# Kernel tuning notes

Measured on AMD Instinct MI355X. Metric: run time of the kernel, lower is better.

## Reference

```python
import jax, jax.numpy as jnp
import numpy as np
from jax import lax

# SLAYER neuron / simulation constants (from netParams)
THETA = 10.0       # spike threshold
TAU_SR = 10.0      # synaptic (PSP) time constant
TAU_REF = 1.0      # refractory time constant
SCALE_REF = 2.0    # refractory scale
TAU_RHO = 1.0      # surrogate-gradient width (unused in fwd)
K_PSP = 32         # truncation length of SRM alpha kernel
K_REF = 16         # truncation length of refractory kernel

_t = np.arange(K_PSP, dtype=np.float64)
PSP_KERN = jnp.asarray((_t / TAU_SR) * np.exp(1.0 - _t / TAU_SR), jnp.float32)  # [K_PSP]
_tr = np.arange(1, K_REF + 1, dtype=np.float64)
REF_KERN = jnp.asarray(-SCALE_REF * THETA * (_tr / TAU_REF) * np.exp(1.0 - _tr / TAU_REF), jnp.float32)  # [K_REF]


def psp(x):
    """Causal temporal FIR filter with SRM alpha kernel; x: [..., T]."""
    sh = x.shape
    T = sh[-1]
    flat = x.reshape(-1, 1, T)                       # [B*, 1, T]
    k = PSP_KERN[::-1][None, None, :]                # correlation kernel (reversed)
    y = lax.conv_general_dilated(flat, k, (1,), [(K_PSP - 1, 0)])
    return y.reshape(sh)


def spike(u):
    """Threshold with refractory feedback, sequential over time. u: [..., T]."""
    uT = jnp.moveaxis(u, -1, 0)                      # [T, ...]
    buf0 = jnp.zeros(u.shape[:-1] + (K_REF,), u.dtype)

    def step(buf, ut):
        v = ut + buf[..., 0]
        s = (v >= THETA).astype(u.dtype)
        buf = jnp.concatenate([buf[..., 1:], jnp.zeros_like(buf[..., :1])], -1)
        buf = buf + s[..., None] * REF_KERN
        return buf, s

    _, sT = lax.scan(step, buf0, uT)
    return jnp.moveaxis(sT, 0, -1)


def conv_t(x, w, stride, pad):
    """2D conv applied independently per timestep. x: [N,C,H,W,T], w: [Co,C,kh,kw]."""
    N, C, H, W, T = x.shape
    xt = jnp.moveaxis(x, -1, 1).reshape(N * T, C, H, W)
    y = lax.conv_general_dilated(xt, w, (stride, stride), [(pad, pad), (pad, pad)])
    Co, Ho, Wo = y.shape[1], y.shape[2], y.shape[3]
    return jnp.moveaxis(y.reshape(N, T, Co, Ho, Wo), 1, -1)


def pool_t(x):
    """SLAYER sum-pool 2x2/s2 with weight 1.1*theta/kernel_area. x: [N,C,H,W,T]."""
    s = lax.reduce_window(x, np.float32(0.0), lax.add, (1, 1, 2, 2, 1), (1, 1, 2, 2, 1), 'VALID')
    return s * np.float32(1.1 * THETA / 4.0)


def setup_inputs() -> dict:
    key = jax.random.key(0)
    ks = jax.random.split(key, 5)
    spikeInput = (jax.random.uniform(ks[0], (4, 2, 256, 256, 50)) < 0.02).astype(jnp.float32)
    w1 = jax.random.normal(ks[1], (8, 2, 5, 5), jnp.float32) * 2.0
    w2 = jax.random.normal(ks[2], (16, 8, 3, 3), jnp.float32) * 1.5
    w3 = jax.random.normal(ks[3], (32, 16, 3, 3), jnp.float32) * 1.5
    w_fc = jax.random.normal(ks[4], (2, 32, 8, 8), jnp.float32) * 0.3
    return {"spikeInput": spikeInput, "w1": w1, "w2": w2, "w3": w3, "w_fc": w_fc}


def reference(spikeInput, w1, w2, w3, w_fc):
    x = spike(conv_t(psp(spikeInput), w1, 2, 1))   # [4,8,127,127,50]
    x = spike(pool_t(psp(x)))                      # [4,8,63,63,50]
    x = spike(conv_t(psp(x), w2, 2, 1))            # [4,16,32,32,50]
    x = spike(pool_t(psp(x)))                      # [4,16,16,16,50]
    x = spike(conv_t(psp(x), w3, 2, 1))            # [4,32,8,8,50]
    u = psp(x)
    out = jnp.einsum('ochw,nchwt->not', w_fc, u)   # dense over (C,H,W)
    return spike(out[:, :, None, None, :])         # [4,2,1,1,50]
```

## Files before the change

### kernel.cpp

```cpp
#include <hip/hip_runtime.h>
#include <cmath>

struct K32 { float k[32]; };
struct K16 { float k[16]; };

#define THETA 10.0f

template <int CIN, int COUT, int KK, int HIN, int WIN, int S1H, int S1W,
          int S2H, int S2W>
__global__ __launch_bounds__(256)
void conv_pps_kernel(const float* __restrict__ x, const float* __restrict__ w,
                     float* __restrict__ s2out, K32 pk, K16 rk) {
  constexpr int WT = 4;
  constexpr int SW = 8;
  constexpr int XR = 2 * (WT - 1) + KK;
  constexpr int GROUPS = (S1W + SW - 1) / SW;
  constexpr int NROW = COUT * 2 * SW;
  constexpr int T0 = 39;
  __shared__ float lds[NROW * 51];
  const int tid = threadIdx.x;
  const int wave = tid >> 6;
  const int lane = tid & 63;
  const int group = blockIdx.x % GROUPS;
  const int rest = blockIdx.x / GROUPS;
  const int hop = rest % S2H;
  const int n = rest / S2H;
  const int ho_off = wave & 1;
  const int wo_half = wave >> 1;
  const int ho = 2 * hop + ho_off;
  const int wo0 = group * SW + wo_half * WT;
  const int tt = lane < 50 ? lane : 49;

  float acc[COUT][WT] = {};
  for (int c = 0; c < CIN; ++c) {
#pragma unroll
    for (int kh = 0; kh < KK; ++kh) {
      const int hi = 2 * ho + kh - 1;
      if ((unsigned)hi >= (unsigned)HIN) continue;
      float xr[XR];
#pragma unroll
      for (int i = 0; i < XR; ++i) {
        const int wi = 2 * wo0 - 1 + i;
        xr[i] = ((unsigned)wi < (unsigned)WIN)
                    ? x[(((size_t)(n * CIN + c) * HIN + hi) * WIN + wi) * 50 + tt]
                    : 0.f;
      }
#pragma unroll
      for (int co = 0; co < COUT; ++co)
#pragma unroll
        for (int kw = 0; kw < KK; ++kw) {
          const float wv = w[((co * CIN + c) * KK + kh) * KK + kw];
#pragma unroll
          for (int wl = 0; wl < WT; ++wl)
            acc[co][wl] += xr[2 * wl + kw] * wv;
        }
    }
  }
  if (lane < 50) {
#pragma unroll
    for (int co = 0; co < COUT; ++co)
#pragma unroll
      for (int wl = 0; wl < WT; ++wl)
        lds[((co * 2 + ho_off) * SW + wo_half * WT + wl) * 51 + lane] = acc[co][wl];
  }
  __syncthreads();
  {
    const int r = tid & (NROW - 1);
    const int part = tid >> 7;
    const int wol = r & (SW - 1);
    const bool act = (group * SW + wol) < S1W;
    float xs[50];
    if (act) {
      if (part == 0) {
#pragma unroll
        for (int t = 0; t < T0; ++t) xs[t] = lds[r * 51 + t];
      } else {
#pragma unroll
        for (int t = 0; t < 50; ++t) xs[t] = lds[r * 51 + t];
      }
    }
    __syncthreads();
    if (act) {
      if (part == 0) {
        float us[T0];
#pragma unroll
        for (int t = 0; t < 32; ++t) {
          float a = 0.f;
#pragma unroll
          for (int k = 31; k >= 0; --k)
            if (t - k >= 0) a += xs[t - k] * pk.k[k];
          us[t] = a;
        }
#pragma unroll
        for (int t = 32; t < T0; ++t) {
          float a = 0.f;
#pragma unroll
          for (int k = 31; k >= 0; --k)
            a += xs[t - k] * pk.k[k];
          us[t] = a;
        }
        float buf[16];
#pragma unroll
        for (int j = 0; j < 16; ++j) buf[j] = 0.f;
#pragma unroll
        for (int t = 0; t < T0; ++t) {
          float v = us[t] + buf[t & 15];
          buf[t & 15] = 0.f;
          float sp = 0.f;
          if (v >= THETA) {
            sp = 1.f;
#pragma unroll
            for (int j = 0; j < 16; ++j) buf[(t + 1 + j) & 15] += rk.k[j];
          }
          us[t] = sp;
        }
#pragma unroll
        for (int t = 0; t < 32; ++t) {
          float a = 0.f;
#pragma unroll
          for (int k = 31; k >= 0; --k)
            if (t - k >= 0) a += us[t - k] * pk.k[k];
          lds[r * 51 + t] = a;
        }
#pragma unroll
        for (int t = 32; t < T0; ++t) {
          float a = 0.f;
#pragma unroll
          for (int k = 31; k >= 0; --k)
            a += us[t - k] * pk.k[k];
          lds[r * 51 + t] = a;
        }
      } else {
        float us[50];
#pragma unroll
        for (int t = 0; t < 32; ++t) {
          float a = 0.f;
#pragma unroll
          for (int k = 31; k >= 0; --k)
            if (t - k >= 0) a += xs[t - k] * pk.k[k];
          us[t] = a;
        }
#pragma unroll
        for (int t = 32; t < 50; ++t) {
          float a = 0.f;
#pragma unroll
          for (int k = 31; k >= 0; --k)
            a += xs[t - k] * pk.k[k];
          us[t] = a;
        }
        float buf[16];
#pragma unroll
        for (int j = 0; j < 16; ++j) buf[j] = 0.f;
#pragma unroll
        for (int t = 0; t < 50; ++t) {
          float v = us[t] + buf[t & 15];
          buf[t & 15] = 0.f;
          float sp = 0.f;
          if (v >= THETA) {
            sp = 1.f;
#pragma unroll
            for (int j = 0; j < 16; ++j) buf[(t + 1 + j) & 15] += rk.k[j];
          }
          us[t] = sp;
        }
#pragma unroll
        for (int t = T0; t < 50; ++t) {
          float a = 0.f;
#pragma unroll
          for (int k = 31; k >= 0; --k)
            a += us[t - k] * pk.k[k];
          lds[r * 51 + t] = a;
        }
      }
    }
  }
  __syncthreads();
  if (tid < COUT * (SW / 2)) {
    const int co = tid / (SW / 2);
    const int wpl = tid % (SW / 2);
    const int wop = group * (SW / 2) + wpl;
    if (wop < S2W) {
      const int r00 = (co * 16 + 2 * wpl) * 51;
      const int r01 = (co * 16 + 2 * wpl + 1) * 51;
      const int r10 = (co * 16 + 8 + 2 * wpl) * 51;
      const int r11 = (co * 16 + 8 + 2 * wpl + 1) * 51;
      float* orow = s2out + (((size_t)(n * COUT + co) * S2H + hop) * S2W + wop) * 50;
      float buf[16];
#pragma unroll
      for (int j = 0; j < 16; ++j) buf[j] = 0.f;
      float prev = 0.f;
#pragma unroll
      for (int t = 0; t < 50; ++t) {
        const float u0 = (((lds[r00 + t] + lds[r01 + t]) + lds[r10 + t]) + lds[r11 + t]) * 2.75f;
        float v = u0 + buf[t & 15];
        buf[t & 15] = 0.f;
        float sp = 0.f;
        if (v >= THETA) {
          sp = 1.f;
#pragma unroll
          for (int j = 0; j < 16; ++j) buf[(t + 1 + j) & 15] += rk.k[j];
        }
        if (t & 1) *(float2*)(orow + t - 1) = make_float2(prev, sp);
        else prev = sp;
      }
    }
  }
}

template <int CIN, int COUT, int KK, int SW, int WT, int HIN, int WIN,
          int S1H, int S1W, int S2H, int S2W>
__global__ __launch_bounds__(256)
void conv_pps2_kernel(const float* __restrict__ x, const float* __restrict__ w,
                      float* __restrict__ s2out, K32 pk, K16 rk) {
  constexpr int XR = 2 * (WT - 1) + KK;
  constexpr int GROUPS = (S1W + SW - 1) / SW;
  constexpr int NROW = COUT * 2 * SW;
  constexpr int NROWP = COUT * (SW / 2);
  __shared__ float lds[NROW * 51];
  const int tid = threadIdx.x;
  const int wave = tid >> 6;
  const int lane = tid & 63;
  const int group = blockIdx.x % GROUPS;
  const int rest = blockIdx.x / GROUPS;
  const int hop = rest % S2H;
  const int n = rest / S2H;
  const int ho_off = wave & 1;
  const int wo_half = wave >> 1;
  const int ho = 2 * hop + ho_off;
  const int wo0 = group * SW + wo_half * WT;
  const int tt = lane < 50 ? lane : 49;

  float acc[COUT][WT] = {};
  for (int c = 0; c < CIN; ++c) {
#pragma unroll
    for (int kh = 0; kh < KK; ++kh) {
      const int hi = 2 * ho + kh - 1;
      if ((unsigned)hi >= (unsigned)HIN) continue;
      float xr[XR];
#pragma unroll
      for (int i = 0; i < XR; ++i) {
        const int wi = 2 * wo0 - 1 + i;
        xr[i] = ((unsigned)wi < (unsigned)WIN)
                    ? x[(((size_t)(n * CIN + c) * HIN + hi) * WIN + wi) * 50 + tt]
                    : 0.f;
      }
#pragma unroll
      for (int co = 0; co < COUT; ++co)
#pragma unroll
        for (int kw = 0; kw < KK; ++kw) {
          const float wv = w[((co * CIN + c) * KK + kh) * KK + kw];
#pragma unroll
          for (int wl = 0; wl < WT; ++wl)
            acc[co][wl] += xr[2 * wl + kw] * wv;
        }
    }
  }
  if (lane < 50) {
#pragma unroll
    for (int co = 0; co < COUT; ++co)
#pragma unroll
      for (int wl = 0; wl < WT; ++wl)
        lds[((co * 2 + ho_off) * SW + wo_half * WT + wl) * 51 + lane] = acc[co][wl];
  }
  __syncthreads();
  {
    const int r = tid & (NROW - 1);
    const int part = tid >> 7;
    float xs[50];
    if (part == 0) {
#pragma unroll
      for (int t = 0; t < 32; ++t) xs[t] = lds[r * 51 + t];
    } else {
#pragma unroll
      for (int t = 0; t < 50; ++t) xs[t] = lds[r * 51 + t];
    }
    __syncthreads();
    if (part == 0) {
#pragma unroll
      for (int t = 0; t < 32; ++t) {
        float a = 0.f;
#pragma unroll
        for (int k = 31; k >= 0; --k)
          if (t - k >= 0) a += xs[t - k] * pk.k[k];
        lds[r * 51 + t] = a;
      }
    } else {
#pragma unroll
      for (int t = 32; t < 50; ++t) {
        float a = 0.f;
#pragma unroll
        for (int k = 31; k >= 0; --k)
          a += xs[t - k] * pk.k[k];
        lds[r * 51 + t] = a;
      }
    }
  }
  __syncthreads();
  if (tid < NROW) {
    float buf[16];
#pragma unroll
    for (int j = 0; j < 16; ++j) buf[j] = 0.f;
#pragma unroll
    for (int t = 0; t < 50; ++t) {
      float v = lds[tid * 51 + t] + buf[t & 15];
      buf[t & 15] = 0.f;
      float sp = 0.f;
      if (v >= THETA) {
        sp = 1.f;
#pragma unroll
        for (int j = 0; j < 16; ++j) buf[(t + 1 + j) & 15] += rk.k[j];
      }
      lds[tid * 51 + t] = sp;
    }
  }
  __syncthreads();
  {
    const int r = tid & (NROWP - 1);
    const int part = tid >> 5;
    const bool act = part < 2;
    const int co = r / (SW / 2);
    const int wpl = r % (SW / 2);
    const int r00 = ((co * 2) * SW + 2 * wpl) * 51;
    const int r01 = r00 + 51;
    const int r10 = ((co * 2 + 1) * SW + 2 * wpl) * 51;
    const int r11 = r10 + 51;
    float xs[50];
    if (act) {
      if (part == 0) {
#pragma unroll
        for (int t = 0; t < 32; ++t)
          xs[t] = (((lds[r00 + t] + lds[r01 + t]) + lds[r10 + t]) + lds[r11 + t]) * 2.75f;
      } else {
#pragma unroll
        for (int t = 0; t < 50; ++t)
          xs[t] = (((lds[r00 + t] + lds[r01 + t]) + lds[r10 + t]) + lds[r11 + t]) * 2.75f;
      }
    }
    __syncthreads();
    if (act) {
      if (part == 0) {
#pragma unroll
        for (int t = 0; t < 32; ++t) {
          float a = 0.f;
#pragma unroll
          for (int k = 31; k >= 0; --k)
            if (t - k >= 0) a += xs[t - k] * pk.k[k];
          lds[r00 + t] = a;
        }
      } else {
#pragma unroll
        for (int t = 32; t < 50; ++t) {
          float a = 0.f;
#pragma unroll
          for (int k = 31; k >= 0; --k)
            a += xs[t - k] * pk.k[k];
          lds[r00 + t] = a;
        }
      }
    }
  }
  __syncthreads();
  if (tid < NROWP) {
    const int co = tid / (SW / 2);
    const int wpl = tid % (SW / 2);
    const int wop = group * (SW / 2) + wpl;
    if (wop < S2W) {
      const int r00 = ((co * 2) * SW + 2 * wpl) * 51;
      float* orow = s2out + (((size_t)(n * COUT + co) * S2H + hop) * S2W + wop) * 50;
      float buf[16];
#pragma unroll
      for (int j = 0; j < 16; ++j) buf[j] = 0.f;
      float prev = 0.f;
#pragma unroll
      for (int t = 0; t < 50; ++t) {
        float v = lds[r00 + t] + buf[t & 15];
        buf[t & 15] = 0.f;
        float sp = 0.f;
        if (v >= THETA) {
          sp = 1.f;
#pragma unroll
          for (int j = 0; j < 16; ++j) buf[(t + 1 + j) & 15] += rk.k[j];
        }
        if (t & 1) *(float2*)(orow + t - 1) = make_float2(prev, sp);
        else prev = sp;
      }
    }
  }
}

template <int CIN, int COUT, int KK, int WT, int HIN, int WIN, int HOUT, int WOUT>
__global__ __launch_bounds__(256)
void conv_fir_spike_kernel(const float* __restrict__ x, const float* __restrict__ w,
                           float* __restrict__ s, K32 pk, K16 rk) {
  constexpr int XR = 2 * (WT - 1) + KK;
  constexpr int TW = 4 * WT;
  constexpr int GROUPS = (WOUT + TW - 1) / TW;
  constexpr int NROW = COUT * TW;
  __shared__ float lds[NROW * 51];
  const int tid = threadIdx.x;
  const int wave = tid >> 6;
  const int lane = tid & 63;
  const int group = blockIdx.x % GROUPS;
  const int rest = blockIdx.x / GROUPS;
  const int ho = rest % HOUT;
  const int n = rest / HOUT;
  const int wo0 = group * TW + wave * WT;
  const int tt = lane < 50 ? lane : 49;

  float acc[COUT][WT] = {};
  for (int c = 0; c < CIN; ++c) {
#pragma unroll
    for (int kh = 0; kh < KK; ++kh) {
      const int hi = 2 * ho + kh - 1;
      if ((unsigned)hi >= (unsigned)HIN) continue;
      float xr[XR];
#pragma unroll
      for (int i = 0; i < XR; ++i) {
        const int wi = 2 * wo0 - 1 + i;
        xr[i] = ((unsigned)wi < (unsigned)WIN)
                    ? x[(((size_t)(n * CIN + c) * HIN + hi) * WIN + wi) * 50 + tt]
                    : 0.f;
      }
#pragma unroll
      for (int co = 0; co < COUT; ++co)
#pragma unroll
        for (int kw = 0; kw < KK; ++kw) {
          const float wv = w[((co * CIN + c) * KK + kh) * KK + kw];
#pragma unroll
          for (int wl = 0; wl < WT; ++wl)
            acc[co][wl] += xr[2 * wl + kw] * wv;
        }
    }
  }

  if (lane < 50) {
#pragma unroll
    for (int co = 0; co < COUT; ++co)
#pragma unroll
      for (int wl = 0; wl < WT; ++wl)
        lds[(co * TW + wave * WT + wl) * 51 + lane] = acc[co][wl];
  }
  __syncthreads();
  {
    const int r = tid % NROW;
    const int part = tid / NROW;
    const int wol = r % TW;
    const bool act = (part < 2) && (group * TW + wol < WOUT);
    float xs[50];
    if (act) {
      if (part == 0) {
#pragma unroll
        for (int t = 0; t < 25; ++t) xs[t] = lds[r * 51 + t];
      } else {
#pragma unroll
        for (int t = 0; t < 50; ++t) xs[t] = lds[r * 51 + t];
      }
    }
    __syncthreads();
    if (act) {
      if (part == 0) {
#pragma unroll
        for (int t = 0; t < 25; ++t) {
          float a = 0.f;
#pragma unroll
          for (int k = 31; k >= 0; --k)
            if (t - k >= 0) a += xs[t - k] * pk.k[k];
          lds[r * 51 + t] = a;
        }
      } else {
#pragma unroll
        for (int t = 25; t < 50; ++t) {
          float a = 0.f;
#pragma unroll
          for (int k = 31; k >= 0; --k)
            if (t - k >= 0) a += xs[t - k] * pk.k[k];
          lds[r * 51 + t] = a;
        }
      }
    }
  }
  __syncthreads();
  if (tid < NROW) {
    const int co = tid / TW;
    const int wol = tid - co * TW;
    const int wo = group * TW + wol;
    if (wo < WOUT) {
      float* orow = s + (((size_t)(n * COUT + co) * HOUT + ho) * WOUT + wo) * 50;
      float buf[16];
#pragma unroll
      for (int j = 0; j < 16; ++j) buf[j] = 0.f;
      float prev = 0.f;
#pragma unroll
      for (int t = 0; t < 50; ++t) {
        float v = lds[tid * 51 + t] + buf[t & 15];
        buf[t & 15] = 0.f;
        float sp = 0.f;
        if (v >= THETA) {
          sp = 1.f;
#pragma unroll
          for (int j = 0; j < 16; ++j) buf[(t + 1 + j) & 15] += rk.k[j];
        }
        if (t & 1) *(float2*)(orow + t - 1) = make_float2(prev, sp);
        else prev = sp;
      }
    }
  }
}

__global__ __launch_bounds__(512)
void fc_fir_spike_kernel(const float* __restrict__ w, const float* __restrict__ s,
                         float* __restrict__ out, K32 pk, K16 rk) {
  __shared__ float lds[8 * 51];
  const int tid = threadIdx.x;
  const int wave = tid >> 6, lane = tid & 63;
  const int o = wave & 1, n = wave >> 1;
  const int tt = lane < 50 ? lane : 49;
  const float* wrow = w + (size_t)o * 2048;
  const float* ub = s + (size_t)n * 2048 * 50;
  float acc = 0.f;
#pragma unroll 32
  for (int i = 0; i < 2048; ++i) acc += wrow[i] * ub[(size_t)i * 50 + tt];
  if (lane < 50) lds[wave * 51 + lane] = acc;
  __syncthreads();
  {
    const int r = tid & 7;
    const int part = tid >> 3;
    const bool act = part < 2;
    float xs[50];
    if (act) {
      if (part == 0) {
#pragma unroll
        for (int t = 0; t < 25; ++t) xs[t] = lds[r * 51 + t];
      } else {
#pragma unroll
        for (int t = 0; t < 50; ++t) xs[t] = lds[r * 51 + t];
      }
    }
    __syncthreads();
    if (act) {
      if (part == 0) {
#pragma unroll
        for (int t = 0; t < 25; ++t) {
          float a = 0.f;
#pragma unroll
          for (int k = 31; k >= 0; --k)
            if (t - k >= 0) a += xs[t - k] * pk.k[k];
          lds[r * 51 + t] = a;
        }
      } else {
#pragma unroll
        for (int t = 25; t < 50; ++t) {
          float a = 0.f;
#pragma unroll
          for (int k = 31; k >= 0; --k)
            if (t - k >= 0) a += xs[t - k] * pk.k[k];
          lds[r * 51 + t] = a;
        }
      }
    }
  }
  __syncthreads();
  if (tid < 8) {
    float buf[16];
#pragma unroll
    for (int j = 0; j < 16; ++j) buf[j] = 0.f;
#pragma unroll
    for (int t = 0; t < 50; ++t) {
      float v = lds[tid * 51 + t] + buf[t & 15];
      buf[t & 15] = 0.f;
      float sp = 0.f;
      if (v >= THETA) {
        sp = 1.f;
#pragma unroll
        for (int j = 0; j < 16; ++j) buf[(t + 1 + j) & 15] += rk.k[j];
      }
      out[tid * 50 + t] = sp;
    }
  }
}

extern "C" void kernel_launch(void* const* d_in, const int* in_sizes, int n_in,
                              void* d_out, int out_size, void* d_ws, size_t ws_size,
                              hipStream_t stream) {
  const float* xin = (const float*)d_in[0];
  const float* w1  = (const float*)d_in[1];
  const float* w2  = (const float*)d_in[2];
  const float* w3  = (const float*)d_in[3];
  const float* wfc = (const float*)d_in[4];
  float* out = (float*)d_out;

  float* R0 = (float*)d_ws;
  float* R1 = R0 + 26214400;

  K32 pk;
  for (int k = 0; k < 32; ++k)
    pk.k[k] = (float)(((double)k / 10.0) * exp(1.0 - (double)k / 10.0));
  K16 rk;
  for (int j = 0; j < 16; ++j) {
    const double tr = (double)(j + 1);
    rk.k[j] = (float)(-2.0 * 10.0 * tr * exp(1.0 - tr));
  }

  conv_pps_kernel<2, 8, 5, 256, 256, 127, 127, 63, 63>
      <<<4 * 63 * 16, 256, 0, stream>>>(xin, w1, R1, pk, rk);
  conv_pps2_kernel<8, 16, 3, 4, 2, 63, 63, 32, 32, 16, 16>
      <<<4 * 16 * 8, 256, 0, stream>>>(R1, w2, R0, pk, rk);
  conv_fir_spike_kernel<16, 32, 3, 1, 16, 16, 8, 8>
      <<<4 * 8 * 2, 256, 0, stream>>>(R0, w3, R1, pk, rk);
  fc_fir_spike_kernel<<<1, 512, 0, stream>>>(wfc, R1, out, pk, rk);
}
```

Baseline: 464.8 us.

## Split time-domain PSP/spike work across two thread halves via spike bitmask handoff

Before, the second thread half redundantly recomputed the full 50-step PSP and spike scan, while the first half handled steps 0-38. Now part 0 computes steps 0-31 and writes its spike bits to shared memory as a packed mask. Part 1 precomputes PSP for steps 32-49 in parallel, then rebuilds the refractory buffer from that mask and finishes the scan and output PSP. This cuts redundant serial work at the cost of an extra barrier and some shared-memory traffic.

```diff
diff --git a/kernel.cpp b/kernel.cpp
--- a/kernel.cpp
+++ b/kernel.cpp
@@ -16,7 +16,6 @@
   constexpr int XR = 2 * (WT - 1) + KK;
   constexpr int GROUPS = (S1W + SW - 1) / SW;
   constexpr int NROW = COUT * 2 * SW;
-  constexpr int T0 = 39;
   __shared__ float lds[NROW * 51];
   const int tid = threadIdx.x;
   const int wave = tid >> 6;
@@ -73,87 +72,82 @@
     if (act) {
       if (part == 0) {
 #pragma unroll
-        for (int t = 0; t < T0; ++t) xs[t] = lds[r * 51 + t];
+        for (int t = 0; t < 32; ++t) xs[t] = lds[r * 51 + t];
       } else {
 #pragma unroll
         for (int t = 0; t < 50; ++t) xs[t] = lds[r * 51 + t];
       }
     }
     __syncthreads();
-    if (act) {
-      if (part == 0) {
-        float us[T0];
+    float s0[32];
+    float u1[18];
+    if (act) {
+      if (part == 0) {
 #pragma unroll
         for (int t = 0; t < 32; ++t) {
           float a = 0.f;
 #pragma unroll
           for (int k = 31; k >= 0; --k)
             if (t - k >= 0) a += xs[t - k] * pk.k[k];
-          us[t] = a;
-        }
-#pragma unroll
-        for (int t = 32; t < T0; ++t) {
-          float a = 0.f;
-#pragma unroll
-          for (int k = 31; k >= 0; --k)
-            a += xs[t - k] * pk.k[k];
-          us[t] = a;
+          s0[t] = a;
         }
         float buf[16];
 #pragma unroll
         for (int j = 0; j < 16; ++j) buf[j] = 0.f;
-#pragma unroll
-        for (int t = 0; t < T0; ++t) {
-          float v = us[t] + buf[t & 15];
+        unsigned bits = 0u;
+#pragma unroll
+        for (int t = 0; t < 32; ++t) {
+          float v = s0[t] + buf[t & 15];
           buf[t & 15] = 0.f;
           float sp = 0.f;
           if (v >= THETA) {
             sp = 1.f;
+            bits |= (1u << t);
 #pragma unroll
             for (int j = 0; j < 16; ++j) buf[(t + 1 + j) & 15] += rk.k[j];
           }
-          us[t] = sp;
-        }
+          s0[t] = sp;
+        }
+        lds[r * 51 + 50] = __uint_as_float(bits);
+      } else {
+#pragma unroll
+        for (int t = 32; t < 50; ++t) {
+          float a = 0.f;
+#pragma unroll
+          for (int k = 31; k >= 0; --k)
+            a += xs[t - k] * pk.k[k];
+          u1[t - 32] = a;
+        }
+      }
+    }
+    __syncthreads();
+    if (act) {
+      if (part == 0) {
 #pragma unroll
         for (int t = 0; t < 32; ++t) {
           float a = 0.f;
 #pragma unroll
           for (int k = 31; k >= 0; --k)
-            if (t - k >= 0) a += us[t - k] * pk.k[k];
+            if (t - k >= 0) a += s0[t - k] * pk.k[k];
           lds[r * 51 + t] = a;
         }
-#pragma unroll
-        for (int t = 32; t < T0; ++t) {
-          float a = 0.f;
-#pragma unroll
-          for (int k = 31; k >= 0; --k)
-            a += us[t - k] * pk.k[k];
-          lds[r * 51 + t] = a;
-        }
-      } else {
-        float us[50];
-#pragma unroll
-        for (int t = 0; t < 32; ++t) {
-          float a = 0.f;
-#pragma unroll
-          for (int k = 31; k >= 0; --k)
-            if (t - k >= 0) a += xs[t - k] * pk.k[k];
-          us[t] = a;
+      } else {
+        const unsigned bits = __float_as_uint(lds[r * 51 + 50]);
+        float sa[50];
+#pragma unroll
+        for (int t = 0; t < 32; ++t) sa[t] = (bits >> t) & 1u ? 1.f : 0.f;
+        float buf[16];
+#pragma unroll
+        for (int d = 0; d < 16; ++d) {
+          float a = 0.f;
+#pragma unroll
+          for (int tau = 16; tau <= 31; ++tau)
+            if (tau >= 16 + d) a += sa[tau] * rk.k[31 + d - tau];
+          buf[d] = a;
         }
 #pragma unroll
         for (int t = 32; t < 50; ++t) {
-          float a = 0.f;
-#pragma unroll
-          for (int k = 31; k >= 0; --k)
-            a += xs[t - k] * pk.k[k];
-          us[t] = a;
-        }
-        float buf[16];
-#pragma unroll
-        for (int j = 0; j < 16; ++j) buf[j] = 0.f;
-#pragma unroll
-        for (int t = 0; t < 50; ++t) {
-          float v = us[t] + buf[t & 15];
+          float v = u1[t - 32] + buf[t & 15];
           buf[t & 15] = 0.f;
           float sp = 0.f;
           if (v >= THETA) {
@@ -161,14 +155,14 @@
 #pragma unroll
             for (int j = 0; j < 16; ++j) buf[(t + 1 + j) & 15] += rk.k[j];
           }
-          us[t] = sp;
-        }
-#pragma unroll
-        for (int t = T0; t < 50; ++t) {
-          float a = 0.f;
-#pragma unroll
-          for (int k = 31; k >= 0; --k)
-            a += us[t - k] * pk.k[k];
+          sa[t] = sp;
+        }
+#pragma unroll
+        for (int t = 32; t < 50; ++t) {
+          float a = 0.f;
+#pragma unroll
+          for (int k = 31; k >= 0; --k)
+            a += sa[t - k] * pk.k[k];
           lds[r * 51 + t] = a;
         }
       }
```

Result: slower. 589.2 us (+26.8%).
